# Kernel tuning notes

Measured on AMD Instinct MI355X. Metric: run time of the kernel, lower is better.

## Reference

```python
import jax, jax.numpy as jnp
import numpy as np

N_COLS = 4096
N_ROWS = 4096
H = 64          # args.hidden1
S = 2           # per-edge supp feature count (cv_supp/vc_supp dim 0)
S_VO = 2        # vo_supp feature dim
S_CO = 2        # co_supp feature dim
EDGE_DENSITY = 0.03


def setup_inputs() -> dict:
    key = jax.random.key(0)
    ks = jax.random.split(key, 20)
    col_hidden = jax.random.normal(ks[0], (N_COLS, H), jnp.float32)
    row_hidden = jax.random.normal(ks[1], (N_ROWS, H), jnp.float32)
    obj_hidden = jax.random.normal(ks[2], (1, H), jnp.float32)
    # sparse bipartite adjacency encoded in supp[0] != 0 (as in the TF code)
    mask = jax.random.bernoulli(ks[3], EDGE_DENSITY, (N_ROWS, N_COLS))
    cv_supp = jax.random.normal(ks[4], (S, N_ROWS, N_COLS), jnp.float32) * mask[None]
    vc_supp = jnp.transpose(cv_supp, (0, 2, 1))  # [S, ncols, nrows]
    vo_supp = jax.random.normal(ks[5], (N_COLS, S_VO), jnp.float32)
    co_supp = jax.random.normal(ks[6], (N_ROWS, S_CO), jnp.float32)
    w = 0.05
    W_vo = jax.random.normal(ks[7], (2 * H, H), jnp.float32) * w
    W_oc = jax.random.normal(ks[8], (2 * H, H), jnp.float32) * w
    W_vc = jax.random.normal(ks[9], (2 * H, H), jnp.float32) * w
    W_co = jax.random.normal(ks[10], (2 * H, H), jnp.float32) * w
    W_ov = jax.random.normal(ks[11], (2 * H, H), jnp.float32) * w
    W_cv = jax.random.normal(ks[12], (2 * H, H), jnp.float32) * w
    # attention scorer nets: Dense(concat_dim -> 1) + sigmoid
    w_attn_vo = jax.random.normal(ks[13], (2 * H + S_VO, 1), jnp.float32) * 0.1
    b_attn_vo = jnp.zeros((), jnp.float32)
    w_attn_co = jax.random.normal(ks[14], (2 * H + S_CO, 1), jnp.float32) * 0.1
    b_attn_co = jnp.zeros((), jnp.float32)
    # pairwise attn nets decomposed into [col | supp | row] weight slices
    w_cv_col = jax.random.normal(ks[15], (H,), jnp.float32) * 0.1
    w_cv_supp = jax.random.normal(ks[16], (S,), jnp.float32) * 0.1
    w_cv_row = jax.random.normal(ks[17], (H,), jnp.float32) * 0.1
    b_cv = jnp.zeros((), jnp.float32)
    w_vc_row = jax.random.normal(ks[18], (H,), jnp.float32) * 0.1
    w_vc_supp = jax.random.normal(ks[19], (S,), jnp.float32) * 0.1
    w_vc_col = jax.random.normal(jax.random.fold_in(key, 99), (H,), jnp.float32) * 0.1
    b_vc = jnp.zeros((), jnp.float32)
    return dict(col_hidden=col_hidden, row_hidden=row_hidden, obj_hidden=obj_hidden,
                cv_supp=cv_supp, vc_supp=vc_supp, vo_supp=vo_supp, co_supp=co_supp,
                W_vo=W_vo, W_oc=W_oc, W_vc=W_vc, W_co=W_co, W_ov=W_ov, W_cv=W_cv,
                w_attn_vo=w_attn_vo, b_attn_vo=b_attn_vo,
                w_attn_co=w_attn_co, b_attn_co=b_attn_co,
                w_cv_col=w_cv_col, w_cv_supp=w_cv_supp, w_cv_row=w_cv_row, b_cv=b_cv,
                w_vc_row=w_vc_row, w_vc_supp=w_vc_supp, w_vc_col=w_vc_col, b_vc=b_vc)


def _forward(col_hidden, row_hidden, obj_hidden, cv_supp, vc_supp, vo_supp, co_supp,
             W_vo, W_oc, W_vc, W_co, W_ov, W_cv,
             w_attn_vo, b_attn_vo, w_attn_co, b_attn_co,
             w_cv_col, w_cv_supp, w_cv_row, b_cv,
             w_vc_row, w_vc_supp, w_vc_col, b_vc):
    act = jax.nn.relu
    ncols, nrows = col_hidden.shape[0], row_hidden.shape[0]
    # ---- v -> o: attend over all columns, update obj node ----
    vo_in = jnp.concatenate([col_hidden, vo_supp,
                             jnp.broadcast_to(obj_hidden, (ncols, H))], axis=1)
    a_vo = jax.nn.sigmoid(vo_in @ w_attn_vo + b_attn_vo)          # [ncols, 1]
    v_o_out = a_vo.T @ col_hidden                                  # [1, H]
    obj = act(jnp.concatenate([obj_hidden, v_o_out], axis=1) @ W_vo)
    # ---- v -> c: per-row ragged neighbor attention, vectorized via masked pairwise scores ----
    nbr_cv = cv_supp[0] != 0                                       # [nrows, ncols]
    logits_cv = ((row_hidden @ w_cv_row)[:, None]
                 + (col_hidden @ w_cv_col)[None, :]
                 + jnp.einsum('snc,s->nc', cv_supp, w_cv_supp) + b_cv)
    score_cv = jnp.where(nbr_cv, jax.nn.sigmoid(logits_cv), 0.0)   # [nrows, ncols]
    v_out = score_cv @ col_hidden                                  # [nrows, H]
    o_c_out = act(jnp.concatenate([jnp.broadcast_to(obj, (nrows, H)), row_hidden], axis=1) @ W_oc)
    row_next = act(jnp.concatenate([o_c_out, v_out], axis=1) @ W_vc)
    # ---- c -> o ----
    co_in = jnp.concatenate([row_next, co_supp,
                             jnp.broadcast_to(obj, (nrows, H))], axis=1)
    a_co = jax.nn.sigmoid(co_in @ w_attn_co + b_attn_co)           # [nrows, 1]
    c_o_out = a_co.T @ row_next                                    # [1, H]
    obj = act(jnp.concatenate([obj, c_o_out], axis=1) @ W_co)
    # ---- c -> v ----
    nbr_vc = vc_supp[0] != 0                                       # [ncols, nrows]
    logits_vc = ((col_hidden @ w_vc_col)[:, None]
                 + (row_next @ w_vc_row)[None, :]
                 + jnp.einsum('scn,s->cn', vc_supp, w_vc_supp) + b_vc)
    score_vc = jnp.where(nbr_vc, jax.nn.sigmoid(logits_vc), 0.0)   # [ncols, nrows]
    c_out = score_vc @ row_next                                    # [ncols, H]
    o_v_out = act(jnp.concatenate([jnp.broadcast_to(obj, (ncols, H)), col_hidden], axis=1) @ W_ov)
    col_next = act(jnp.concatenate([o_v_out, c_out], axis=1) @ W_cv)
    return col_next, row_next, obj


def reference(col_hidden, row_hidden, obj_hidden, cv_supp, vc_supp, vo_supp, co_supp,
              W_vo, W_oc, W_vc, W_co, W_ov, W_cv,
              w_attn_vo, b_attn_vo, w_attn_co, b_attn_co,
              w_cv_col, w_cv_supp, w_cv_row, b_cv,
              w_vc_row, w_vc_supp, w_vc_col, b_vc):
    col_next, row_next, obj = _forward(
        col_hidden, row_hidden, obj_hidden, cv_supp, vc_supp, vo_supp, co_supp,
        W_vo, W_oc, W_vc, W_co, W_ov, W_cv,
        w_attn_vo, b_attn_vo, w_attn_co, b_attn_co,
        w_cv_col, w_cv_supp, w_cv_row, b_cv,
        w_vc_row, w_vc_supp, w_vc_col, b_vc)
    # original layer also passes the supp tensors through unchanged
    return (col_next, row_next, obj, cv_supp, vc_supp, vo_supp, co_supp)
```

## Files before the change

kernel.cpp:

```cpp
#include <hip/hip_runtime.h>
#include <math.h>

typedef float f4  __attribute__((ext_vector_type(4)));
typedef short s8v __attribute__((ext_vector_type(8)));
typedef unsigned short u16;
typedef u16 us4 __attribute__((ext_vector_type(4)));

#define PLANE (4096*4096)

#define OUT_COL 0
#define OUT_ROW 262144
#define OUT_OBJ 524288
#define OUT_CV  524352
#define OUT_VC  34078784
#define OUT_VO  67633216
#define OUT_CO  67641408

#define WS_VO_P  0
#define WS_CO_P  1024
#define WS_OBJ1  2048
#define WS_RDCV  2112
#define WS_CDCV  6208
#define WS_RDVC  10304
#define WS_CDVC  14400
#define WS_GPART 18496
#define WS_SC    2115648
#define WS_BT1   10504256
#define WS_BT2   10635328

__device__ __forceinline__ float sigf(float x) {
    return 1.0f / (1.0f + __expf(-x));
}
__device__ __forceinline__ u16 f2bf(float x) {
    unsigned u = __float_as_uint(x);
    return (u16)((u + 0x7FFFu + ((u >> 16) & 1u)) >> 16);
}

__device__ __forceinline__ void transpose_tile(int k0, int t,
    const float* __restrict__ X, u16* __restrict__ BT, float* lds )
{
    #pragma unroll
    for (int it = 0; it < 4; ++it) {
        const int idx = it * 256 + t;
        const int r = idx >> 4, c4 = (idx & 15) * 4;
        f4 v = *(const f4*)(X + (size_t)(k0 + r) * 64 + c4);
        *(f4*)(lds + r * 72 + c4) = v;
    }
    __syncthreads();
    #pragma unroll
    for (int it = 0; it < 4; ++it) {
        const int idx = it * 256 + t;
        const int h = idx >> 4, q = (idx & 15) * 4;
        us4 o;
        o.x = f2bf(lds[(q + 0) * 72 + h]);
        o.y = f2bf(lds[(q + 1) * 72 + h]);
        o.z = f2bf(lds[(q + 2) * 72 + h]);
        o.w = f2bf(lds[(q + 3) * 72 + h]);
        *(us4*)(BT + (size_t)h * 4096 + k0 + q) = o;
    }
}

__device__ __forceinline__ void attn_body(
    int blk, int t, const float* __restrict__ X, const float* __restrict__ supp,
    const float* __restrict__ obj, const float* __restrict__ wat,
    const float* __restrict__ bat, float* __restrict__ accP,
    const float* __restrict__ wextra, float* __restrict__ dextra,
    float* sA, float* sAcc)
{
    const int i = blk * 256 + t;
    float od = 0.f;
    for (int h = 0; h < 64; ++h) od += obj[h] * wat[66 + h];
    float x = bat[0] + od + supp[i*2] * wat[64] + supp[i*2+1] * wat[65];
    const f4* Xr = (const f4*)(X + i*64);
    f4 xd = 0.f, dd = 0.f;
    #pragma unroll
    for (int q = 0; q < 16; ++q) {
        f4 xv = Xr[q];
        xd += xv * ((const f4*)wat)[q];
        if (wextra) dd += xv * ((const f4*)wextra)[q];
    }
    x += xd.x + xd.y + xd.z + xd.w;
    if (dextra) dextra[i] = dd.x + dd.y + dd.z + dd.w;
    sA[t] = sigf(x);
    if (t < 64) sAcc[t] = 0.f;
    __syncthreads();
    const int w = t >> 6, h = t & 63;
    const int base = blk * 256 + w * 64;
    float partial = 0.f;
    for (int j = 0; j < 64; ++j)
        partial += sA[w*64 + j] * X[(base + j)*64 + h];
    atomicAdd(&sAcc[h], partial);
    __syncthreads();
    if (t < 64) accP[blk*64 + t] = sAcc[t];
}

__global__ __launch_bounds__(256) void k_front(
    const float* __restrict__ col_hidden, const float* __restrict__ row_hidden,
    const float* __restrict__ w_cv_col, const float* __restrict__ w_vc_col,
    const float* __restrict__ w_cv_row,
    float* __restrict__ cdcv, float* __restrict__ cdvc, float* __restrict__ rdcv,
    const float* __restrict__ vo_supp, const float* __restrict__ co_supp,
    float* __restrict__ out_vo, float* __restrict__ out_co,
    const float* __restrict__ obj_hidden, const float* __restrict__ w_attn_vo,
    const float* __restrict__ b_attn_vo, float* __restrict__ voP,
    u16* __restrict__ BT1)
{
    __shared__ float sA[256];
    __shared__ float sAcc[64];
    __shared__ float tr[64*72];
    const int t = threadIdx.x;
    if (blockIdx.x < 3072) {
        const int gw = blockIdx.x * 4 + (t >> 6);
        const int lane = t & 63;
        const int which = gw >> 12;
        const int row = gw & 4095;
        const float* x; const float* w; float* dst;
        if (which == 0)      { x = col_hidden; w = w_cv_col; dst = cdcv; }
        else if (which == 1) { x = col_hidden; w = w_vc_col; dst = cdvc; }
        else                 { x = row_hidden; w = w_cv_row; dst = rdcv; }
        float v = x[row * 64 + lane] * w[lane];
        #pragma unroll
        for (int off = 32; off; off >>= 1) v += __shfl_down(v, off, 64);
        if (lane == 0) dst[row] = v;
        return;
    }
    if (blockIdx.x < 3088) {
        const int idx = (blockIdx.x - 3072) * 256 + t;
        if (idx < 2048) ((f4*)out_vo)[idx] = ((const f4*)vo_supp)[idx];
        else            ((f4*)out_co)[idx - 2048] = ((const f4*)co_supp)[idx - 2048];
        return;
    }
    if (blockIdx.x < 3104) {
        attn_body(blockIdx.x - 3088, t, col_hidden, vo_supp, obj_hidden,
                  w_attn_vo, b_attn_vo, voP, nullptr, nullptr, sA, sAcc);
        return;
    }
    transpose_tile((blockIdx.x - 3104) * 64, t, col_hidden, BT1, tr);
}

__global__ __launch_bounds__(256) void k_attn(
    const float* __restrict__ X, const float* __restrict__ supp,
    const float* __restrict__ obj, const float* __restrict__ wat,
    const float* __restrict__ bat, float* __restrict__ accP,
    const float* __restrict__ wextra, float* __restrict__ dextra,
    u16* __restrict__ BT2)
{
    __shared__ float sA[256];
    __shared__ float sAcc[64];
    __shared__ float tr[64*72];
    if (blockIdx.x < 16) {
        attn_body(blockIdx.x, threadIdx.x, X, supp, obj, wat, bat, accP,
                  wextra, dextra, sA, sAcc);
        return;
    }
    transpose_tile((blockIdx.x - 16) * 64, threadIdx.x, X, BT2, tr);
}

__global__ __launch_bounds__(256, 8) void k_stream(
    const float* __restrict__ supp0, const float* __restrict__ supp1,
    const float* __restrict__ perrow, const float* __restrict__ percol,
    const float* __restrict__ wsup, const float* __restrict__ bias,
    float* __restrict__ pass0, float* __restrict__ pass1,
    u16* __restrict__ score)
{
    const float w0 = wsup[0], w1 = wsup[1], bv = bias[0];
    const int N4 = PLANE / 4;
    const int stride = gridDim.x * 256;
    for (int idx = blockIdx.x * 256 + threadIdx.x; idx < N4; idx += stride) {
        const int row = idx >> 10;
        const int j0  = (idx & 1023) * 4;
        f4 a0 = ((const f4*)supp0)[idx];
        f4 a1 = ((const f4*)supp1)[idx];
        __builtin_nontemporal_store(a0, (f4*)pass0 + idx);
        __builtin_nontemporal_store(a1, (f4*)pass1 + idx);
        const float rd = perrow[row];
        f4 cd = *(const f4*)(percol + j0);
        f4 lg = rd + cd + w0 * a0 + w1 * a1 + bv;
        us4 o;
        o.x = (a0.x != 0.f) ? f2bf(sigf(lg.x)) : (u16)0;
        o.y = (a0.y != 0.f) ? f2bf(sigf(lg.y)) : (u16)0;
        o.z = (a0.z != 0.f) ? f2bf(sigf(lg.z)) : (u16)0;
        o.w = (a0.w != 0.f) ? f2bf(sigf(lg.w)) : (u16)0;
        ((us4*)score)[idx] = o;
    }
}

__global__ __launch_bounds__(256, 4) void k_gemm(
    const u16* __restrict__ sc, const u16* __restrict__ BT,
    float* __restrict__ part,
    const float* __restrict__ objL, const float* __restrict__ objRp,
    const float* __restrict__ Wobj, float* __restrict__ objDst)
{
    __shared__ float rsum[64];
    const int t = threadIdx.x;
    if (blockIdx.x == 512) {
        if (t < 64) {
            float r = 0.f;
            for (int b = 0; b < 16; ++b) r += objRp[b*64 + t];
            rsum[t] = r;
        }
        __syncthreads();
        if (t < 64) {
            float acc = 0.f;
            for (int k = 0; k < 64; ++k) acc += objL[k] * Wobj[k*64 + t];
            for (int k = 0; k < 64; ++k) acc += rsum[k] * Wobj[(64+k)*64 + t];
            objDst[t] = fmaxf(acc, 0.f);
        }
        return;
    }
    const int mblk = blockIdx.x >> 3;
    const int ks   = blockIdx.x & 7;
    const int wv   = t >> 6, lane = t & 63;
    const int i0   = mblk * 64 + wv * 16;
    const int m    = lane & 15, quad = lane >> 4;
    const int k0   = ks * 512;

    f4 acc0 = 0.f, acc1 = 0.f, acc2 = 0.f, acc3 = 0.f;
    const u16* ap  = sc + (size_t)(i0 + m) * 4096 + k0 + quad * 8;
    const u16* bp  = BT + (size_t)m * 4096 + k0 + quad * 8;
    #pragma unroll 4
    for (int kc = 0; kc < 512; kc += 32) {
        s8v a  = *(const s8v*)(ap + kc);
        s8v b0 = *(const s8v*)(bp + kc);
        s8v b1 = *(const s8v*)(bp + 16 * 4096 + kc);
        s8v b2 = *(const s8v*)(bp + 32 * 4096 + kc);
        s8v b3 = *(const s8v*)(bp + 48 * 4096 + kc);
        acc0 = __builtin_amdgcn_mfma_f32_16x16x32_bf16(a, b0, acc0, 0, 0, 0);
        acc1 = __builtin_amdgcn_mfma_f32_16x16x32_bf16(a, b1, acc1, 0, 0, 0);
        acc2 = __builtin_amdgcn_mfma_f32_16x16x32_bf16(a, b2, acc2, 0, 0, 0);
        acc3 = __builtin_amdgcn_mfma_f32_16x16x32_bf16(a, b3, acc3, 0, 0, 0);
    }
    float* pb = part + (size_t)ks * 262144;
    #pragma unroll
    for (int r = 0; r < 4; ++r) {
        const size_t ro = (size_t)(i0 + quad * 4 + r) * 64 + m;
        pb[ro +  0] = acc0[r];
        pb[ro + 16] = acc1[r];
        pb[ro + 32] = acc2[r];
        pb[ro + 48] = acc3[r];
    }
}

__global__ __launch_bounds__(256) void k_mlp2(
    const float* __restrict__ objx, const float* __restrict__ base,
    const float* __restrict__ W1, const float* __restrict__ part,
    const float* __restrict__ W2, float* __restrict__ dst)
{
    __shared__ float mid[4][64];
    __shared__ float accs[4][64];
    const int t = threadIdx.x, w = t >> 6, h = t & 63;
    const int n = blockIdx.x * 4 + w;
    float v = 0.f;
    #pragma unroll
    for (int j = 0; j < 8; ++j) v += part[(size_t)j * 262144 + n*64 + h];
    accs[w][h] = v;
    float m = 0.f;
    for (int k = 0; k < 64; ++k) m += objx[k] * W1[k*64 + h];
    for (int k = 0; k < 64; ++k) m += base[n*64 + k] * W1[(64+k)*64 + h];
    mid[w][h] = fmaxf(m, 0.f);
    __syncthreads();
    float o = 0.f;
    for (int k = 0; k < 64; ++k) o += mid[w][k] * W2[k*64 + h];
    for (int k = 0; k < 64; ++k) o += accs[w][k] * W2[(64+k)*64 + h];
    dst[n*64 + h] = fmaxf(o, 0.f);
}

extern "C" void kernel_launch(void* const* d_in, const int* in_sizes, int n_in,
                              void* d_out, int out_size, void* d_ws, size_t ws_size,
                              hipStream_t stream)
{
    const float* col_hidden = (const float*)d_in[0];
    const float* row_hidden = (const float*)d_in[1];
    const float* obj_hidden = (const float*)d_in[2];
    const float* cv_supp    = (const float*)d_in[3];
    const float* vc_supp    = (const float*)d_in[4];
    const float* vo_supp    = (const float*)d_in[5];
    const float* co_supp    = (const float*)d_in[6];
    const float* W_vo       = (const float*)d_in[7];
    const float* W_oc       = (const float*)d_in[8];
    const float* W_vc       = (const float*)d_in[9];
    const float* W_co       = (const float*)d_in[10];
    const float* W_ov       = (const float*)d_in[11];
    const float* W_cv       = (const float*)d_in[12];
    const float* w_attn_vo  = (const float*)d_in[13];
    const float* b_attn_vo  = (const float*)d_in[14];
    const float* w_attn_co  = (const float*)d_in[15];
    const float* b_attn_co  = (const float*)d_in[16];
    const float* w_cv_col   = (const float*)d_in[17];
    const float* w_cv_supp  = (const float*)d_in[18];
    const float* w_cv_row   = (const float*)d_in[19];
    const float* b_cv       = (const float*)d_in[20];
    const float* w_vc_row   = (const float*)d_in[21];
    const float* w_vc_supp  = (const float*)d_in[22];
    const float* w_vc_col   = (const float*)d_in[23];
    const float* b_vc       = (const float*)d_in[24];

    float* out = (float*)d_out;
    float* ws  = (float*)d_ws;
    u16* SC  = (u16*)(ws + WS_SC);
    u16* BT1 = (u16*)(ws + WS_BT1);
    u16* BT2 = (u16*)(ws + WS_BT2);

    k_front<<<3168, 256, 0, stream>>>(col_hidden, row_hidden, w_cv_col, w_vc_col, w_cv_row,
                                      ws + WS_CDCV, ws + WS_CDVC, ws + WS_RDCV,
                                      vo_supp, co_supp, out + OUT_VO, out + OUT_CO,
                                      obj_hidden, w_attn_vo, b_attn_vo, ws + WS_VO_P, BT1);
    k_stream<<<4096, 256, 0, stream>>>(cv_supp, cv_supp + PLANE,
                                       ws + WS_RDCV, ws + WS_CDCV, w_cv_supp, b_cv,
                                       out + OUT_CV, out + OUT_CV + PLANE, SC);
    k_gemm<<<513, 256, 0, stream>>>(SC, BT1, ws + WS_GPART,
                                    obj_hidden, ws + WS_VO_P, W_vo, ws + WS_OBJ1);
    k_mlp2<<<1024, 256, 0, stream>>>(ws + WS_OBJ1, row_hidden, W_oc, ws + WS_GPART, W_vc,
                                     out + OUT_ROW);
    k_attn<<<80, 256, 0, stream>>>(out + OUT_ROW, co_supp, ws + WS_OBJ1, w_attn_co,
                                   b_attn_co, ws + WS_CO_P, w_vc_row, ws + WS_RDVC, BT2);
    k_stream<<<4096, 256, 0, stream>>>(vc_supp, vc_supp + PLANE,
                                       ws + WS_CDVC, ws + WS_RDVC, w_vc_supp, b_vc,
                                       out + OUT_VC, out + OUT_VC + PLANE, SC);
    k_gemm<<<513, 256, 0, stream>>>(SC, BT2, ws + WS_GPART,
                                    ws + WS_OBJ1, ws + WS_CO_P, W_co, out + OUT_OBJ);
    k_mlp2<<<1024, 256, 0, stream>>>(out + OUT_OBJ, col_hidden, W_ov, ws + WS_GPART, W_cv,
                                     out + OUT_COL);
}
```

Measured before the change: 588.5 us.

## Split pass-through copy from scoring and fuse row dot into MLP epilogue

Moves the supp pass-through copies for both directions into a single dedicated copy kernel. The two streaming kernels become score-only kernels with one block per row and no grid-stride loop. The per-row vc dot product moves from the attention kernel into the first MLP kernel's epilogue using a wavefront reduction. This simplifies the streaming kernels and lets the copy run as one large launch, but the supp planes are now read twice, adding memory traffic.

Measured after the change: 647.1 us. 1.1x slower.

```diff
diff --git a/kernel.cpp b/kernel.cpp
--- a/kernel.cpp
+++ b/kernel.cpp
@@ -64,7 +64,6 @@
     int blk, int t, const float* __restrict__ X, const float* __restrict__ supp,
     const float* __restrict__ obj, const float* __restrict__ wat,
     const float* __restrict__ bat, float* __restrict__ accP,
-    const float* __restrict__ wextra, float* __restrict__ dextra,
     float* sA, float* sAcc)
 {
     const int i = blk * 256 + t;
@@ -72,15 +71,10 @@
     for (int h = 0; h < 64; ++h) od += obj[h] * wat[66 + h];
     float x = bat[0] + od + supp[i*2] * wat[64] + supp[i*2+1] * wat[65];
     const f4* Xr = (const f4*)(X + i*64);
-    f4 xd = 0.f, dd = 0.f;
-    #pragma unroll
-    for (int q = 0; q < 16; ++q) {
-        f4 xv = Xr[q];
-        xd += xv * ((const f4*)wat)[q];
-        if (wextra) dd += xv * ((const f4*)wextra)[q];
-    }
+    f4 xd = 0.f;
+    #pragma unroll
+    for (int q = 0; q < 16; ++q) xd += Xr[q] * ((const f4*)wat)[q];
     x += xd.x + xd.y + xd.z + xd.w;
-    if (dextra) dextra[i] = dd.x + dd.y + dd.z + dd.w;
     sA[t] = sigf(x);
     if (t < 64) sAcc[t] = 0.f;
     __syncthreads();
@@ -132,7 +126,7 @@
     }
     if (blockIdx.x < 3104) {
         attn_body(blockIdx.x - 3088, t, col_hidden, vo_supp, obj_hidden,
-                  w_attn_vo, b_attn_vo, voP, nullptr, nullptr, sA, sAcc);
+                  w_attn_vo, b_attn_vo, voP, sA, sAcc);
         return;
     }
     transpose_tile((blockIdx.x - 3104) * 64, t, col_hidden, BT1, tr);
@@ -142,38 +136,48 @@
     const float* __restrict__ X, const float* __restrict__ supp,
     const float* __restrict__ obj, const float* __restrict__ wat,
     const float* __restrict__ bat, float* __restrict__ accP,
-    const float* __restrict__ wextra, float* __restrict__ dextra,
     u16* __restrict__ BT2)
 {
     __shared__ float sA[256];
     __shared__ float sAcc[64];
     __shared__ float tr[64*72];
     if (blockIdx.x < 16) {
-        attn_body(blockIdx.x, threadIdx.x, X, supp, obj, wat, bat, accP,
-                  wextra, dextra, sA, sAcc);
+        attn_body(blockIdx.x, threadIdx.x, X, supp, obj, wat, bat, accP, sA, sAcc);
         return;
     }
     transpose_tile((blockIdx.x - 16) * 64, threadIdx.x, X, BT2, tr);
 }
 
-__global__ __launch_bounds__(256, 8) void k_stream(
+__global__ __launch_bounds__(256) void k_copy(
+    const float* __restrict__ a, const float* __restrict__ b,
+    float* __restrict__ da, float* __restrict__ db)
+{
+    const int t = threadIdx.x;
+    const f4* src; f4* dst; size_t off;
+    if (blockIdx.x < 8192) { src = (const f4*)a; dst = (f4*)da; off = (size_t)blockIdx.x * 1024; }
+    else                   { src = (const f4*)b; dst = (f4*)db; off = (size_t)(blockIdx.x - 8192) * 1024; }
+    #pragma unroll
+    for (int it = 0; it < 4; ++it) {
+        const size_t i = off + t + it * 256;
+        dst[i] = src[i];
+    }
+}
+
+__global__ __launch_bounds__(256) void k_score(
     const float* __restrict__ supp0, const float* __restrict__ supp1,
     const float* __restrict__ perrow, const float* __restrict__ percol,
     const float* __restrict__ wsup, const float* __restrict__ bias,
-    float* __restrict__ pass0, float* __restrict__ pass1,
     u16* __restrict__ score)
 {
     const float w0 = wsup[0], w1 = wsup[1], bv = bias[0];
-    const int N4 = PLANE / 4;
-    const int stride = gridDim.x * 256;
-    for (int idx = blockIdx.x * 256 + threadIdx.x; idx < N4; idx += stride) {
-        const int row = idx >> 10;
-        const int j0  = (idx & 1023) * 4;
+    const float rd = perrow[blockIdx.x];
+    const size_t base = (size_t)blockIdx.x * 1024 + threadIdx.x;
+    #pragma unroll
+    for (int it = 0; it < 4; ++it) {
+        const size_t idx = base + it * 256;
+        const int j0 = (int)(idx & 1023) * 4;
         f4 a0 = ((const f4*)supp0)[idx];
         f4 a1 = ((const f4*)supp1)[idx];
-        __builtin_nontemporal_store(a0, (f4*)pass0 + idx);
-        __builtin_nontemporal_store(a1, (f4*)pass1 + idx);
-        const float rd = perrow[row];
         f4 cd = *(const f4*)(percol + j0);
         f4 lg = rd + cd + w0 * a0 + w1 * a1 + bv;
         us4 o;
@@ -244,7 +248,8 @@
 __global__ __launch_bounds__(256) void k_mlp2(
     const float* __restrict__ objx, const float* __restrict__ base,
     const float* __restrict__ W1, const float* __restrict__ part,
-    const float* __restrict__ W2, float* __restrict__ dst)
+    const float* __restrict__ W2, float* __restrict__ dst,
+    const float* __restrict__ wvcrow, float* __restrict__ rdvc)
 {
     __shared__ float mid[4][64];
     __shared__ float accs[4][64];
@@ -262,7 +267,14 @@
     float o = 0.f;
     for (int k = 0; k < 64; ++k) o += mid[w][k] * W2[k*64 + h];
     for (int k = 0; k < 64; ++k) o += accs[w][k] * W2[(64+k)*64 + h];
-    dst[n*64 + h] = fmaxf(o, 0.f);
+    o = fmaxf(o, 0.f);
+    dst[n*64 + h] = o;
+    if (rdvc) {
+        float rv = o * wvcrow[h];
+        #pragma unroll
+        for (int off = 32; off; off >>= 1) rv += __shfl_down(rv, off, 64);
+        if (h == 0) rdvc[n] = rv;
+    }
 }
 
 extern "C" void kernel_launch(void* const* d_in, const int* in_sizes, int n_in,
@@ -305,20 +317,19 @@
                                       ws + WS_CDCV, ws + WS_CDVC, ws + WS_RDCV,
                                       vo_supp, co_supp, out + OUT_VO, out + OUT_CO,
                                       obj_hidden, w_attn_vo, b_attn_vo, ws + WS_VO_P, BT1);
-    k_stream<<<4096, 256, 0, stream>>>(cv_supp, cv_supp + PLANE,
-                                       ws + WS_RDCV, ws + WS_CDCV, w_cv_supp, b_cv,
-                                       out + OUT_CV, out + OUT_CV + PLANE, SC);
+    k_copy<<<16384, 256, 0, stream>>>(cv_supp, vc_supp, out + OUT_CV, out + OUT_VC);
+    k_score<<<4096, 256, 0, stream>>>(cv_supp, cv_supp + PLANE,
+                                      ws + WS_RDCV, ws + WS_CDCV, w_cv_supp, b_cv, SC);
     k_gemm<<<513, 256, 0, stream>>>(SC, BT1, ws + WS_GPART,
                                     obj_hidden, ws + WS_VO_P, W_vo, ws + WS_OBJ1);
     k_mlp2<<<1024, 256, 0, stream>>>(ws + WS_OBJ1, row_hidden, W_oc, ws + WS_GPART, W_vc,
-                                     out + OUT_ROW);
+                                     out + OUT_ROW, w_vc_row, ws + WS_RDVC);
     k_attn<<<80, 256, 0, stream>>>(out + OUT_ROW, co_supp, ws + WS_OBJ1, w_attn_co,
-                                   b_attn_co, ws + WS_CO_P, w_vc_row, ws + WS_RDVC, BT2);
-    k_stream<<<4096, 256, 0, stream>>>(vc_supp, vc_supp + PLANE,
-                                       ws + WS_CDVC, ws + WS_RDVC, w_vc_supp, b_vc,
-                                       out + OUT_VC, out + OUT_VC + PLANE, SC);
+                                   b_attn_co, ws + WS_CO_P, BT2);
+    k_score<<<4096, 256, 0, stream>>>(vc_supp, vc_supp + PLANE,
+                                      ws + WS_CDVC, ws + WS_RDVC, w_vc_supp, b_vc, SC);
     k_gemm<<<513, 256, 0, stream>>>(SC, BT2, ws + WS_GPART,
                                     ws + WS_OBJ1, ws + WS_CO_P, W_co, out + OUT_OBJ);
     k_mlp2<<<1024, 256, 0, stream>>>(out + OUT_OBJ, col_hidden, W_ov, ws + WS_GPART, W_cv,
-                                     out + OUT_COL);
-}
+                                     out + OUT_COL, nullptr, nullptr);
+}
```
